# Kernel optimization log

Measured on AMD Instinct MI355X. Metric: run time of the kernel, lower is better.

Reference implementation:

```python
import jax, jax.numpy as jnp
import numpy as np

D_MODEL = 1024
D_HEAD = 128


def setup_inputs() -> dict:
    key = jax.random.key(0)
    kx, kq, kk, kv, ko = jax.random.split(key, 5)
    x = jax.random.normal(kx, (4, 2048, D_MODEL), dtype=jnp.float32)
    # xavier-uniform-ish init scale
    s_in = (6.0 / (D_MODEL + D_HEAD)) ** 0.5
    wq = jax.random.uniform(kq, (D_MODEL, D_HEAD), minval=-s_in, maxval=s_in, dtype=jnp.float32)
    wk = jax.random.uniform(kk, (D_MODEL, D_HEAD), minval=-s_in, maxval=s_in, dtype=jnp.float32)
    wv = jax.random.uniform(kv, (D_MODEL, D_HEAD), minval=-s_in, maxval=s_in, dtype=jnp.float32)
    wo = jax.random.uniform(ko, (D_HEAD, D_MODEL), minval=-s_in, maxval=s_in, dtype=jnp.float32)
    return {"x": x, "wq": wq, "wk": wk, "wv": wv, "wo": wo}


def reference(x, wq, wk, wv, wo):
    # x: [b, s, d_model]
    s = x.shape[1]
    scale = 1.0 / (D_HEAD ** 0.5)
    q = jnp.einsum('bsd,dh->bsh', x, wq)
    k = jnp.einsum('bsd,dh->bsh', x, wk)
    v = jnp.einsum('bsd,dh->bsh', x, wv)
    scores = jnp.einsum('bqh,bkh->bqk', q, k) * scale  # [b, s, s]
    causal = jnp.tril(jnp.ones((s, s), dtype=bool))
    scores = jnp.where(causal, scores, -jnp.inf)
    attn = jax.nn.softmax(scores, axis=-1)
    ctx = jnp.einsum('bqk,bkh->bqh', attn, v)
    return jnp.einsum('bsh,hd->bsd', ctx, wo)
```

## Files before the change

kernel.cpp:

```cpp
#include <hip/hip_runtime.h>
#include <hip/hip_bf16.h>
#include <math.h>

typedef _Float16 half8 __attribute__((ext_vector_type(8)));
typedef _Float16 half4_t __attribute__((ext_vector_type(4)));
typedef _Float16 half2_t __attribute__((ext_vector_type(2)));
typedef float floatx4 __attribute__((ext_vector_type(4)));
typedef float floatx2 __attribute__((ext_vector_type(2)));

#define MFMA16(a, b, c) __builtin_amdgcn_mfma_f32_16x16x32_f16(a, b, c, 0, 0, 0)
#define MASKVAL (-30000.0f)
#define QSCALE 0.1275261529f

__global__ __launch_bounds__(256) void wprep(
    const float* __restrict__ wq, const float* __restrict__ wk,
    const float* __restrict__ wv, const float* __restrict__ wo,
    _Float16* __restrict__ wqt, _Float16* __restrict__ wkt,
    _Float16* __restrict__ wvt, _Float16* __restrict__ wot) {
  __shared__ float T[32][36];
  int bx = blockIdx.x, tid = threadIdx.x;
  const float* src;
  _Float16* dst;
  int R, C, r0, c0;
  float sc = 1.0f;
  if (bx < 384) {
    int p = bx >> 7, t = bx & 127;
    src = (p == 0) ? wq : (p == 1) ? wk : wv;
    dst = (p == 0) ? wqt : (p == 1) ? wkt : wvt;
    if (p == 0) sc = QSCALE;
    R = 1024; C = 128;
    r0 = (t & 31) * 32; c0 = (t >> 5) * 32;
  } else {
    int t = bx - 384;
    src = wo; dst = wot;
    R = 128; C = 1024;
    r0 = (t & 3) * 32; c0 = (t >> 2) * 32;
  }
  {
    int row = tid >> 3, c4 = (tid & 7) * 4;
    float4 f = *(const float4*)&src[(size_t)(r0 + row) * C + c0 + c4];
    T[row][c4] = f.x; T[row][c4 + 1] = f.y; T[row][c4 + 2] = f.z; T[row][c4 + 3] = f.w;
  }
  __syncthreads();
  {
    int cc = tid >> 3, r4 = (tid & 7) * 4;
    half4_t h;
    h[0] = (_Float16)(T[r4 + 0][cc] * sc);
    h[1] = (_Float16)(T[r4 + 1][cc] * sc);
    h[2] = (_Float16)(T[r4 + 2][cc] * sc);
    h[3] = (_Float16)(T[r4 + 3][cc] * sc);
    *(half4_t*)&dst[(size_t)(c0 + cc) * R + r0 + r4] = h;
  }
}

__global__ __launch_bounds__(256, 3) void qkv_gemm(
    const float* __restrict__ x, const _Float16* __restrict__ wqt,
    const _Float16* __restrict__ wkt, const _Float16* __restrict__ wvt,
    _Float16* __restrict__ Qh, _Float16* __restrict__ Kh,
    _Float16* __restrict__ Vt) {
  __shared__ _Float16 A_lds[32 * 136];
  __shared__ _Float16 B_lds[128 * 136];
  int tid = threadIdx.x;
  int w = tid >> 6, lane = tid & 63, quad = lane >> 4, l16 = lane & 15;
  int m0 = blockIdx.x * 32;
  int proj = blockIdx.y;
  const _Float16* wt = (proj == 0) ? wqt : (proj == 1) ? wkt : wvt;
  floatx4 zero = {0.f, 0.f, 0.f, 0.f};
  floatx4 acc[2][2];
#pragma unroll
  for (int mi = 0; mi < 2; mi++)
#pragma unroll
    for (int ni = 0; ni < 2; ni++) acc[mi][ni] = zero;

  int arow = tid >> 3, ac0 = (tid & 7) * 16;
  int brow = tid >> 1, bc0 = (tid & 1) * 64;
  int nw = w * 32;

  const float* asrc = x + (size_t)(m0 + arow) * 1024 + ac0;
  const _Float16* bsrc = wt + (size_t)brow * 1024 + bc0;

  float4 af[4];
  half8 bf[8];
#pragma unroll
  for (int i = 0; i < 4; i++) af[i] = ((const float4*)asrc)[i];
#pragma unroll
  for (int i = 0; i < 8; i++) bf[i] = ((const half8*)bsrc)[i];

  for (int k0 = 0; k0 < 1024; k0 += 128) {
    {
      half8 h0, h1;
      h0[0] = (_Float16)af[0].x; h0[1] = (_Float16)af[0].y;
      h0[2] = (_Float16)af[0].z; h0[3] = (_Float16)af[0].w;
      h0[4] = (_Float16)af[1].x; h0[5] = (_Float16)af[1].y;
      h0[6] = (_Float16)af[1].z; h0[7] = (_Float16)af[1].w;
      h1[0] = (_Float16)af[2].x; h1[1] = (_Float16)af[2].y;
      h1[2] = (_Float16)af[2].z; h1[3] = (_Float16)af[2].w;
      h1[4] = (_Float16)af[3].x; h1[5] = (_Float16)af[3].y;
      h1[6] = (_Float16)af[3].z; h1[7] = (_Float16)af[3].w;
      *(half8*)&A_lds[arow * 136 + ac0] = h0;
      *(half8*)&A_lds[arow * 136 + ac0 + 8] = h1;
    }
#pragma unroll
    for (int i = 0; i < 8; i++)
      *(half8*)&B_lds[brow * 136 + bc0 + i * 8] = bf[i];
    __syncthreads();

    if (k0 + 128 < 1024) {
      const float* a2 = asrc + k0 + 128;
      const _Float16* b2 = bsrc + k0 + 128;
#pragma unroll
      for (int i = 0; i < 4; i++) af[i] = ((const float4*)a2)[i];
#pragma unroll
      for (int i = 0; i < 8; i++) bf[i] = ((const half8*)b2)[i];
    }

    half8 a[2][4];
#pragma unroll
    for (int c = 0; c < 4; c++) {
      a[0][c] = *(const half8*)&A_lds[l16 * 136 + c * 32 + quad * 8];
      a[1][c] = *(const half8*)&A_lds[(16 + l16) * 136 + c * 32 + quad * 8];
    }
#pragma unroll
    for (int ni = 0; ni < 2; ni++)
#pragma unroll
      for (int c = 0; c < 4; c++) {
        half8 b = *(const half8*)&B_lds[(nw + ni * 16 + l16) * 136 + c * 32 + quad * 8];
        acc[0][ni] = MFMA16(a[0][c], b, acc[0][ni]);
        acc[1][ni] = MFMA16(a[1][c], b, acc[1][ni]);
      }
    __syncthreads();
  }
  if (proj < 2) {
#pragma unroll
    for (int mi = 0; mi < 2; mi++)
#pragma unroll
      for (int ni = 0; ni < 2; ni++)
#pragma unroll
        for (int r = 0; r < 4; r++) {
          int row = m0 + mi * 16 + quad * 4 + r;
          int col = nw + ni * 16 + l16;
          _Float16 v = (_Float16)acc[mi][ni][r];
          if (proj == 0) Qh[(size_t)row * 128 + col] = v;
          else           Kh[(size_t)row * 128 + col] = v;
        }
  } else {
    _Float16* Vl = B_lds;
#pragma unroll
    for (int mi = 0; mi < 2; mi++)
#pragma unroll
      for (int ni = 0; ni < 2; ni++)
#pragma unroll
        for (int r = 0; r < 4; r++) {
          int lrow = mi * 16 + quad * 4 + r;
          int col = nw + ni * 16 + l16;
          Vl[col * 40 + lrow] = (_Float16)acc[mi][ni][r];
        }
    __syncthreads();
    int col = tid >> 1, hh = tid & 1;
    int bb = m0 >> 11, s0 = (m0 & 2047) + hh * 16;
    half8 h0 = *(half8*)&Vl[col * 40 + hh * 16];
    half8 h1 = *(half8*)&Vl[col * 40 + hh * 16 + 8];
    _Float16* dstv = Vt + ((size_t)(bb * 128 + col)) * 2048 + s0;
    *(half8*)&dstv[0] = h0;
    *(half8*)&dstv[8] = h1;
  }
}

__global__ __launch_bounds__(256, 3) void attn_partial(
    const _Float16* __restrict__ Qh, const _Float16* __restrict__ Kh,
    const _Float16* __restrict__ Vt, _Float16* __restrict__ Opart,
    float* __restrict__ Ml) {
  __shared__ _Float16 KV_lds[128 * 136];
  __shared__ _Float16 P_lds[4 * 16 * 136];
  int tid = threadIdx.x;
  int w = tid >> 6, lane = tid & 63, quad = lane >> 4, l16 = lane & 15;
  int g = (int)blockIdx.x;
  int b = g & 3;
  int r = g >> 2;
  int m = (int)sqrtf((float)r * 0.5f);
  while (2 * m * (m + 1) > r) m--;
  while (2 * (m + 1) * (m + 2) <= r) m++;
  int r0_ = r - 2 * m * (m + 1);
  int qdiv = r0_ / (m + 1);
  int qt = 4 * m + qdiv;
  int kc = r0_ - qdiv * (m + 1);
  int q0 = qt * 64, k0 = kc * 256;
  int kmax = (qt + 1) * 64;
  int len = kmax - k0; if (len > 256) len = 256;
  int nsub = (len + 127) >> 7;
  int qw0 = q0 + w * 16;
  int sidx = (b * 32 + qt) * 8 + kc;

  const _Float16* Kb = Kh + (size_t)b * 2048 * 128;
  const _Float16* Vb = Vt + (size_t)b * 128 * 2048;

  half8 aq[4];
  {
    const _Float16* qbase = Qh + (size_t)(b * 2048 + qw0 + l16) * 128;
#pragma unroll
    for (int c = 0; c < 4; c++) aq[c] = *(const half8*)&qbase[c * 32 + quad * 8];
  }

  int srow = tid >> 1, scol = (tid & 1) * 64;
  floatx4 zero = {0.f, 0.f, 0.f, 0.f};
  floatx4 O[8];
#pragma unroll
  for (int t = 0; t < 8; t++) O[t] = zero;
  float m_r[4] = {MASKVAL, MASKVAL, MASKVAL, MASKVAL};
  float l_r[4] = {0.f, 0.f, 0.f, 0.f};

  for (int s = 0; s < nsub; s++) {
    int ks = k0 + s * 128;
    if (s) __syncthreads();
#pragma unroll
    for (int i = 0; i < 8; i++)
      *(half8*)&KV_lds[srow * 136 + scol + i * 8] =
          *(const half8*)&Kb[(size_t)(ks + srow) * 128 + scol + i * 8];
    half8 vreg[8];
#pragma unroll
    for (int i = 0; i < 8; i++)
      vreg[i] = *(const half8*)&Vb[(size_t)srow * 2048 + ks + scol + i * 8];
    __syncthreads();

    floatx4 sa[8];
#pragma unroll
    for (int t = 0; t < 8; t++) sa[t] = zero;
#pragma unroll
    for (int t = 0; t < 8; t++)
#pragma unroll
      for (int c = 0; c < 4; c++) {
        half8 bk = *(const half8*)&KV_lds[(t * 16 + l16) * 136 + c * 32 + quad * 8];
        sa[t] = MFMA16(aq[c], bk, sa[t]);
      }

    float sc[4];
#pragma unroll
    for (int j = 0; j < 4; j++) {
      int query = qw0 + quad * 4 + j;
      float mx = MASKVAL;
#pragma unroll
      for (int t = 0; t < 8; t++) {
        float v = (ks + t * 16 + l16 > query) ? MASKVAL : sa[t][j];
        sa[t][j] = v;
        mx = fmaxf(mx, v);
      }
#pragma unroll
      for (int off = 1; off < 16; off <<= 1) mx = fmaxf(mx, __shfl_xor(mx, off));
      float mnew = fmaxf(m_r[j], mx);
      float scj = exp2f(m_r[j] - mnew);
      float rs = 0.f;
#pragma unroll
      for (int t = 0; t < 8; t++) {
        float e = exp2f(sa[t][j] - mnew);
        sa[t][j] = e;
        rs += e;
      }
#pragma unroll
      for (int off = 1; off < 16; off <<= 1) rs += __shfl_xor(rs, off);
      l_r[j] = l_r[j] * scj + rs;
      m_r[j] = mnew;
      sc[j] = scj;
    }
#pragma unroll
    for (int t = 0; t < 8; t++)
#pragma unroll
      for (int j = 0; j < 4; j++) O[t][j] *= sc[j];

    __syncthreads();
#pragma unroll
    for (int i = 0; i < 8; i++)
      *(half8*)&KV_lds[srow * 136 + scol + i * 8] = vreg[i];
    _Float16* P = P_lds + w * 16 * 136;
#pragma unroll
    for (int j = 0; j < 4; j++)
#pragma unroll
      for (int t = 0; t < 8; t++)
        P[(quad * 4 + j) * 136 + t * 16 + l16] = (_Float16)sa[t][j];
    __syncthreads();

#pragma unroll
    for (int c2 = 0; c2 < 4; c2++) {
      half8 ap = *(const half8*)&P[l16 * 136 + c2 * 32 + quad * 8];
#pragma unroll
      for (int t = 0; t < 8; t++) {
        half8 bv = *(const half8*)&KV_lds[(t * 16 + l16) * 136 + c2 * 32 + quad * 8];
        O[t] = MFMA16(ap, bv, O[t]);
      }
    }
  }

  size_t obase = (size_t)sidx * 8192;
#pragma unroll
  for (int t = 0; t < 8; t++)
#pragma unroll
    for (int j = 0; j < 4; j++)
      Opart[obase + (size_t)(w * 16 + quad * 4 + j) * 128 + t * 16 + l16] = (_Float16)O[t][j];
  if (l16 == 0)
#pragma unroll
    for (int j = 0; j < 4; j++) {
      int row = w * 16 + quad * 4 + j;
      floatx2 ml;
      ml[0] = m_r[j];
      ml[1] = l_r[j];
      *(floatx2*)&Ml[(size_t)sidx * 128 + row * 2] = ml;
    }
}

__global__ __launch_bounds__(256) void combine_out(
    const _Float16* __restrict__ Opart, const float* __restrict__ Ml,
    const _Float16* __restrict__ wot, float* __restrict__ out) {
  __shared__ _Float16 A_lds[32 * 136];
  __shared__ _Float16 B_lds[128 * 136];
  int tid = threadIdx.x;
  int r0 = blockIdx.x * 32;
  int b = r0 >> 11, s0 = r0 & 2047;
  int qt = s0 >> 6, rbase = s0 & 63;
  int nkc = (qt + 4) >> 2;
  int sidx0 = (b * 32 + qt) * 8;

  {
    int lr = tid >> 3, c0 = (tid & 7) * 16;
    int ri = rbase + lr;
    float mv[8], lv[8];
#pragma unroll
    for (int i = 0; i < 8; i++) {
      if (i < nkc) {
        floatx2 ml = *(const floatx2*)&Ml[(size_t)(sidx0 + i) * 128 + ri * 2];
        mv[i] = ml[0]; lv[i] = ml[1];
      } else { mv[i] = MASKVAL; lv[i] = 0.f; }
    }
    float M = MASKVAL;
#pragma unroll
    for (int i = 0; i < 8; i++) M = fmaxf(M, mv[i]);
    float L = 0.f;
    float a0[16];
#pragma unroll
    for (int c = 0; c < 16; c++) a0[c] = 0.f;
#pragma unroll
    for (int i = 0; i < 8; i++) {
      if (i < nkc) {
        float scv = exp2f(mv[i] - M);
        L += lv[i] * scv;
        const _Float16* op = &Opart[(size_t)(sidx0 + i) * 8192 + (size_t)ri * 128 + c0];
        half8 o0 = *(const half8*)&op[0];
        half8 o1 = *(const half8*)&op[8];
#pragma unroll
        for (int c = 0; c < 8; c++) {
          a0[c]     += scv * (float)o0[c];
          a0[8 + c] += scv * (float)o1[c];
        }
      }
    }
    float inv = 1.f / L;
    half8 h0, h1;
#pragma unroll
    for (int c = 0; c < 8; c++) {
      h0[c] = (_Float16)(a0[c] * inv);
      h1[c] = (_Float16)(a0[8 + c] * inv);
    }
    *(half8*)&A_lds[lr * 136 + c0] = h0;
    *(half8*)&A_lds[lr * 136 + c0 + 8] = h1;
  }

  int w = tid >> 6, lane = tid & 63, quad = lane >> 4, l16 = lane & 15;
  int bn = tid >> 1, bk = (tid & 1) * 64;
  half8 bf[8];
#pragma unroll
  for (int i = 0; i < 8; i++)
    bf[i] = *(const half8*)&wot[(size_t)bn * 128 + bk + i * 8];
  __syncthreads();

  half8 a[2][4];
#pragma unroll
  for (int c = 0; c < 4; c++) {
    a[0][c] = *(const half8*)&A_lds[l16 * 136 + c * 32 + quad * 8];
    a[1][c] = *(const half8*)&A_lds[(16 + l16) * 136 + c * 32 + quad * 8];
  }
  floatx4 zero = {0.f, 0.f, 0.f, 0.f};
  for (int nc = 0; nc < 8; nc++) {
#pragma unroll
    for (int i = 0; i < 8; i++)
      *(half8*)&B_lds[bn * 136 + bk + i * 8] = bf[i];
    __syncthreads();
    if (nc < 7) {
#pragma unroll
      for (int i = 0; i < 8; i++)
        bf[i] = *(const half8*)&wot[(size_t)((nc + 1) * 128 + bn) * 128 + bk + i * 8];
    }
    floatx4 acc[2][2];
#pragma unroll
    for (int mi = 0; mi < 2; mi++)
#pragma unroll
      for (int ni = 0; ni < 2; ni++) acc[mi][ni] = zero;
    int nw = w * 32;
#pragma unroll
    for (int ni = 0; ni < 2; ni++)
#pragma unroll
      for (int c = 0; c < 4; c++) {
        half8 bb = *(const half8*)&B_lds[(nw + ni * 16 + l16) * 136 + c * 32 + quad * 8];
        acc[0][ni] = MFMA16(a[0][c], bb, acc[0][ni]);
        acc[1][ni] = MFMA16(a[1][c], bb, acc[1][ni]);
      }
#pragma unroll
    for (int mi = 0; mi < 2; mi++)
#pragma unroll
      for (int ni = 0; ni < 2; ni++)
#pragma unroll
        for (int r = 0; r < 4; r++) {
          int row = r0 + mi * 16 + quad * 4 + r;
          out[(size_t)row * 1024 + nc * 128 + nw + ni * 16 + l16] = acc[mi][ni][r];
        }
    __syncthreads();
  }
}

extern "C" void kernel_launch(void* const* d_in, const int* in_sizes, int n_in,
                              void* d_out, int out_size, void* d_ws, size_t ws_size,
                              hipStream_t stream) {
  const float* x = (const float*)d_in[0];
  const float* wq = (const float*)d_in[1];
  const float* wk = (const float*)d_in[2];
  const float* wv = (const float*)d_in[3];
  const float* wo = (const float*)d_in[4];
  char* ws = (char*)d_ws;
  _Float16* wqt = (_Float16*)(ws + 0);
  _Float16* wkt = (_Float16*)(ws + 262144);
  _Float16* wvt = (_Float16*)(ws + 524288);
  _Float16* wot = (_Float16*)(ws + 786432);
  _Float16* Qh  = (_Float16*)(ws + 1048576);
  _Float16* Kh  = (_Float16*)(ws + 3145728);
  _Float16* Vt  = (_Float16*)(ws + 5242880);
  _Float16* Opart = (_Float16*)(ws + 9437184);
  float* Ml = (float*)(ws + 26214400);
  float* out = (float*)d_out;

  wprep<<<512, 256, 0, stream>>>(wq, wk, wv, wo, wqt, wkt, wvt, wot);
  qkv_gemm<<<dim3(256, 3), 256, 0, stream>>>(x, wqt, wkt, wvt, Qh, Kh, Vt);
  attn_partial<<<576, 256, 0, stream>>>(Qh, Kh, Vt, Opart, Ml);
  combine_out<<<256, 256, 0, stream>>>(Opart, Ml, wot, out);
}
```

Before: 157.2 us.

## Fuse Q, K, V projections into one GEMM kernel sharing the x tile

```diff
diff --git a/kernel.cpp b/kernel.cpp
--- a/kernel.cpp
+++ b/kernel.cpp
@@ -53,109 +53,103 @@
   }
 }
 
-__global__ __launch_bounds__(256, 3) void qkv_gemm(
+__global__ __launch_bounds__(512, 4) void qkv_fused(
     const float* __restrict__ x, const _Float16* __restrict__ wqt,
     const _Float16* __restrict__ wkt, const _Float16* __restrict__ wvt,
     _Float16* __restrict__ Qh, _Float16* __restrict__ Kh,
     _Float16* __restrict__ Vt) {
-  __shared__ _Float16 A_lds[32 * 136];
-  __shared__ _Float16 B_lds[128 * 136];
+  __shared__ _Float16 A_lds[32 * 72];
+  __shared__ _Float16 B_lds[384 * 72];
   int tid = threadIdx.x;
   int w = tid >> 6, lane = tid & 63, quad = lane >> 4, l16 = lane & 15;
   int m0 = blockIdx.x * 32;
-  int proj = blockIdx.y;
-  const _Float16* wt = (proj == 0) ? wqt : (proj == 1) ? wkt : wvt;
   floatx4 zero = {0.f, 0.f, 0.f, 0.f};
-  floatx4 acc[2][2];
+  floatx4 acc[2][3];
 #pragma unroll
   for (int mi = 0; mi < 2; mi++)
 #pragma unroll
-    for (int ni = 0; ni < 2; ni++) acc[mi][ni] = zero;
-
-  int arow = tid >> 3, ac0 = (tid & 7) * 16;
-  int brow = tid >> 1, bc0 = (tid & 1) * 64;
-  int nw = w * 32;
+    for (int ni = 0; ni < 3; ni++) acc[mi][ni] = zero;
+
+  int arow = tid >> 4, ac0 = (tid & 15) * 4;
+  int brow = tid >> 2, bc0 = (tid & 3) * 16;
 
   const float* asrc = x + (size_t)(m0 + arow) * 1024 + ac0;
-  const _Float16* bsrc = wt + (size_t)brow * 1024 + bc0;
-
-  float4 af[4];
-  half8 bf[8];
-#pragma unroll
-  for (int i = 0; i < 4; i++) af[i] = ((const float4*)asrc)[i];
-#pragma unroll
-  for (int i = 0; i < 8; i++) bf[i] = ((const half8*)bsrc)[i];
-
-  for (int k0 = 0; k0 < 1024; k0 += 128) {
+  const _Float16* bsrc0 = wqt + (size_t)brow * 1024 + bc0;
+  const _Float16* bsrc1 = wkt + (size_t)brow * 1024 + bc0;
+  const _Float16* bsrc2 = wvt + (size_t)brow * 1024 + bc0;
+
+  float4 af;
+  half8 bf[3][2];
+  af = *(const float4*)asrc;
+#pragma unroll
+  for (int i = 0; i < 2; i++) {
+    bf[0][i] = *(const half8*)(bsrc0 + i * 8);
+    bf[1][i] = *(const half8*)(bsrc1 + i * 8);
+    bf[2][i] = *(const half8*)(bsrc2 + i * 8);
+  }
+
+  for (int k0 = 0; k0 < 1024; k0 += 64) {
     {
-      half8 h0, h1;
-      h0[0] = (_Float16)af[0].x; h0[1] = (_Float16)af[0].y;
-      h0[2] = (_Float16)af[0].z; h0[3] = (_Float16)af[0].w;
-      h0[4] = (_Float16)af[1].x; h0[5] = (_Float16)af[1].y;
-      h0[6] = (_Float16)af[1].z; h0[7] = (_Float16)af[1].w;
-      h1[0] = (_Float16)af[2].x; h1[1] = (_Float16)af[2].y;
-      h1[2] = (_Float16)af[2].z; h1[3] = (_Float16)af[2].w;
-      h1[4] = (_Float16)af[3].x; h1[5] = (_Float16)af[3].y;
-      h1[6] = (_Float16)af[3].z; h1[7] = (_Float16)af[3].w;
-      *(half8*)&A_lds[arow * 136 + ac0] = h0;
-      *(half8*)&A_lds[arow * 136 + ac0 + 8] = h1;
-    }
-#pragma unroll
-    for (int i = 0; i < 8; i++)
-      *(half8*)&B_lds[brow * 136 + bc0 + i * 8] = bf[i];
-    __syncthreads();
-
-    if (k0 + 128 < 1024) {
-      const float* a2 = asrc + k0 + 128;
-      const _Float16* b2 = bsrc + k0 + 128;
-#pragma unroll
-      for (int i = 0; i < 4; i++) af[i] = ((const float4*)a2)[i];
-#pragma unroll
-      for (int i = 0; i < 8; i++) bf[i] = ((const half8*)b2)[i];
-    }
-
-    half8 a[2][4];
-#pragma unroll
-    for (int c = 0; c < 4; c++) {
-      a[0][c] = *(const half8*)&A_lds[l16 * 136 + c * 32 + quad * 8];
-      a[1][c] = *(const half8*)&A_lds[(16 + l16) * 136 + c * 32 + quad * 8];
-    }
-#pragma unroll
-    for (int ni = 0; ni < 2; ni++)
-#pragma unroll
-      for (int c = 0; c < 4; c++) {
-        half8 b = *(const half8*)&B_lds[(nw + ni * 16 + l16) * 136 + c * 32 + quad * 8];
-        acc[0][ni] = MFMA16(a[0][c], b, acc[0][ni]);
-        acc[1][ni] = MFMA16(a[1][c], b, acc[1][ni]);
-      }
-    __syncthreads();
-  }
-  if (proj < 2) {
+      half4_t h;
+      h[0] = (_Float16)af.x; h[1] = (_Float16)af.y;
+      h[2] = (_Float16)af.z; h[3] = (_Float16)af.w;
+      *(half4_t*)&A_lds[arow * 72 + ac0] = h;
+    }
+#pragma unroll
+    for (int p = 0; p < 3; p++)
+#pragma unroll
+      for (int i = 0; i < 2; i++)
+        *(half8*)&B_lds[(p * 128 + brow) * 72 + bc0 + i * 8] = bf[p][i];
+    __syncthreads();
+
+    if (k0 + 64 < 1024) {
+      af = *(const float4*)(asrc + k0 + 64);
+#pragma unroll
+      for (int i = 0; i < 2; i++) {
+        bf[0][i] = *(const half8*)(bsrc0 + k0 + 64 + i * 8);
+        bf[1][i] = *(const half8*)(bsrc1 + k0 + 64 + i * 8);
+        bf[2][i] = *(const half8*)(bsrc2 + k0 + 64 + i * 8);
+      }
+    }
+
+    half8 a[2][2];
 #pragma unroll
     for (int mi = 0; mi < 2; mi++)
 #pragma unroll
-      for (int ni = 0; ni < 2; ni++)
-#pragma unroll
-        for (int r = 0; r < 4; r++) {
-          int row = m0 + mi * 16 + quad * 4 + r;
-          int col = nw + ni * 16 + l16;
-          _Float16 v = (_Float16)acc[mi][ni][r];
-          if (proj == 0) Qh[(size_t)row * 128 + col] = v;
-          else           Kh[(size_t)row * 128 + col] = v;
-        }
-  } else {
-    _Float16* Vl = B_lds;
-#pragma unroll
-    for (int mi = 0; mi < 2; mi++)
-#pragma unroll
-      for (int ni = 0; ni < 2; ni++)
-#pragma unroll
-        for (int r = 0; r < 4; r++) {
-          int lrow = mi * 16 + quad * 4 + r;
-          int col = nw + ni * 16 + l16;
-          Vl[col * 40 + lrow] = (_Float16)acc[mi][ni][r];
-        }
-    __syncthreads();
+      for (int kc = 0; kc < 2; kc++)
+        a[mi][kc] = *(const half8*)&A_lds[(mi * 16 + l16) * 72 + kc * 32 + quad * 8];
+    int nw = w * 48;
+#pragma unroll
+    for (int ni = 0; ni < 3; ni++)
+#pragma unroll
+      for (int kc = 0; kc < 2; kc++) {
+        half8 b = *(const half8*)&B_lds[(nw + ni * 16 + l16) * 72 + kc * 32 + quad * 8];
+        acc[0][ni] = MFMA16(a[0][kc], b, acc[0][ni]);
+        acc[1][ni] = MFMA16(a[1][kc], b, acc[1][ni]);
+      }
+    __syncthreads();
+  }
+
+  _Float16* Vl = B_lds;
+#pragma unroll
+  for (int mi = 0; mi < 2; mi++)
+#pragma unroll
+    for (int ni = 0; ni < 3; ni++) {
+      int nb = w * 48 + ni * 16;
+#pragma unroll
+      for (int r = 0; r < 4; r++) {
+        int row = m0 + mi * 16 + quad * 4 + r;
+        _Float16 v = (_Float16)acc[mi][ni][r];
+        if (nb < 128)
+          Qh[(size_t)row * 128 + nb + l16] = v;
+        else if (nb < 256)
+          Kh[(size_t)row * 128 + nb - 128 + l16] = v;
+        else
+          Vl[(nb - 256 + l16) * 40 + mi * 16 + quad * 4 + r] = v;
+      }
+    }
+  __syncthreads();
+  if (tid < 256) {
     int col = tid >> 1, hh = tid & 1;
     int bb = m0 >> 11, s0 = (m0 & 2047) + hh * 16;
     half8 h0 = *(half8*)&Vl[col * 40 + hh * 16];
@@ -435,7 +429,7 @@
   float* out = (float*)d_out;
 
   wprep<<<512, 256, 0, stream>>>(wq, wk, wv, wo, wqt, wkt, wvt, wot);
-  qkv_gemm<<<dim3(256, 3), 256, 0, stream>>>(x, wqt, wkt, wvt, Qh, Kh, Vt);
+  qkv_fused<<<256, 512, 0, stream>>>(x, wqt, wkt, wvt, Qh, Kh, Vt);
   attn_partial<<<576, 256, 0, stream>>>(Qh, Kh, Vt, Opart, Ml);
   combine_out<<<256, 256, 0, stream>>>(Opart, Ml, wot, out);
 }
```

Result: faster. 147.7 us, median of 2 (-6.0%).
